# Kernel tuning notes

Measured on AMD Instinct MI355X. Metric: run time of the kernel, lower is better.

The kernel has to match this reference:

```python
import jax, jax.numpy as jnp
import numpy as np

EPS_MAG = 1e-6    # magnitude threshold for valid trajectory
EPS_WSUM = 1e-8   # clamp on combined weight sum


def setup_inputs() -> dict:
    key = jax.random.key(0)
    embeddings = jax.random.normal(key, (4, 4096, 1024), dtype=jnp.float32)
    return {"embeddings": embeddings, "max_trajectory_distance": 8}


def reference(embeddings, max_trajectory_distance):
    # Vectorized form of compute_sparse_trajectories:
    # for each pos p >= 1, window of diffs d[start..p-1], start = max(0, p - max_dist),
    # normalized diffs weighted by linspace(0.1, 1.0, window) * tanh(2*|d|),
    # output[p] = weighted sum / clamp(weight sum, 1e-8); output[0] = 0.
    B, S, D = embeddings.shape
    maxd = min(int(max_trajectory_distance), S - 1)

    d = embeddings[:, 1:, :] - embeddings[:, :-1, :]            # [B, S-1, D]
    mag = jnp.linalg.norm(d, axis=-1)                           # [B, S-1]
    normed = jnp.where((mag > EPS_MAG)[..., None],
                       d / jnp.maximum(mag, EPS_MAG)[..., None],
                       0.0)                                     # [B, S-1, D]
    magw = jnp.tanh(mag * 2.0)                                  # [B, S-1]

    p = jnp.arange(S)                                           # positions
    wsize = jnp.minimum(maxd, p)                                # window size per pos
    j = jnp.arange(maxd)
    idx = p[:, None] - maxd + j[None, :]                        # [S, maxd] diff indices (end-aligned)
    valid = idx >= 0                                            # [S, maxd]
    # k = rank within window (0..wsize-1): weights linspace(0.1, 1.0, wsize)
    k = (j[None, :] - (maxd - wsize)[:, None]).astype(jnp.float32)
    denom = jnp.maximum(wsize - 1, 1).astype(jnp.float32)[:, None]
    lin = jnp.where(wsize[:, None] > 1, 0.1 + 0.9 * k / denom, 0.1)
    lin = jnp.where(valid, lin, 0.0)                            # [S, maxd]

    ci = jnp.clip(idx, 0, S - 2)                                # safe gather indices
    n_g = normed[:, ci, :]                                      # [B, S, maxd, D]
    m_g = magw[:, ci]                                           # [B, S, maxd]
    comb = lin[None, :, :] * m_g * valid[None, :, :]            # combined weights

    wsum = jnp.maximum(comb.sum(axis=-1), EPS_WSUM)             # [B, S]
    traj = jnp.einsum('bsjd,bsj->bsd', n_g, comb) / wsum[..., None]
    return traj
```

## Files before the change

### kernel.cpp

```cpp
#include <hip/hip_runtime.h>
#include <hip/hip_bf16.h>


constexpr int B_ = 4;
constexpr int S_ = 4096;
constexpr int D_ = 1024;
constexpr int MAXD  = 8;
constexpr int CHUNK = 32;
constexpr int ROWS  = CHUNK + MAXD;
constexpr int NDIFF = ROWS - 1;
constexpr int NCH   = S_ / CHUNK;
constexpr int NWG   = B_ * NCH;
constexpr int NXCD  = 8;

typedef float fx4 __attribute__((ext_vector_type(4)));

template <int CTRL, int ROW_MASK>
__device__ __forceinline__ float dpp_add(float x) {
    const int t = __builtin_amdgcn_update_dpp(0, __float_as_int(x),
                                              CTRL, ROW_MASK, 0xf, false);
    return x + __int_as_float(t);
}

__device__ __forceinline__ float wave_reduce_dpp(float x) {
    x = dpp_add<0x111, 0xf>(x);
    x = dpp_add<0x112, 0xf>(x);
    x = dpp_add<0x114, 0xf>(x);
    x = dpp_add<0x118, 0xf>(x);
    x = dpp_add<0x142, 0xa>(x);
    x = dpp_add<0x143, 0xc>(x);
    return x;
}

__global__ __launch_bounds__(256, 2)
void traj_splat_kernel(const float* __restrict__ emb, float* __restrict__ out) {
    const int bid = blockIdx.x;
    const int lin = (bid % NXCD) * (NWG / NXCD) + bid / NXCD;
    const int schunk = lin & (NCH - 1);
    const int b      = lin >> 7;

    const int s0   = schunk * CHUNK;
    const int lane = threadIdx.x & 63;
    const int wave = threadIdx.x >> 6;
    const int d0   = threadIdx.x * 4;

    const float* __restrict__ embB = emb + (size_t)b * S_ * D_;

    __shared__ float part[NDIFF][5];
    __shared__ float smagw[NDIFF];
    __shared__ float sq[NDIFF];
    __shared__ float gco[CHUNK][12];

    float4 win[ROWS];
    #pragma unroll
    for (int r = 0; r < ROWS; ++r) {
        const int row = s0 - MAXD + r;
        win[r] = (row >= 0) ? *(const float4*)(embB + (size_t)row * D_ + d0)
                            : make_float4(0.f, 0.f, 0.f, 0.f);
    }

    #pragma unroll
    for (int li = 0; li < NDIFF; ++li) {
        const float4 a = win[li], c = win[li + 1];
        const float dx = c.x - a.x, dy = c.y - a.y;
        const float dz = c.z - a.z, dw = c.w - a.w;
        float sum = dx * dx + dy * dy + dz * dz + dw * dw;
        sum = wave_reduce_dpp(sum);
        if (lane == 63) part[li][wave] = sum;
    }
    __syncthreads();

    if (threadIdx.x < NDIFF) {
        const int li = threadIdx.x;
        const float s2 = part[li][0] + part[li][1] + part[li][2] + part[li][3];
        const float mag = sqrtf(s2);
        const float mw  = tanhf(2.f * mag);
        smagw[li] = mw;
        sq[li]    = (mag > 1e-6f) ? (mw / mag) : 0.f;
    }
    __syncthreads();

    if (threadIdx.x < CHUNK) {
        const int sl = threadIdx.x;
        const int s  = s0 + sl;
        const int ws = min(MAXD, s);
        const int lo = MAXD - ws;
        const float rden = 0.9f / (float)max(ws - 1, 1);

        float cpad[MAXD + 2];
        #pragma unroll
        for (int t = 0; t < MAXD + 2; ++t) cpad[t] = 0.f;

        float wsum = 0.f;
        #pragma unroll
        for (int j = 0; j < MAXD; ++j) {
            if (j >= lo) {
                const int li = sl + j;
                const float lin2 = (ws > 1) ? (0.1f + rden * (float)(j - lo)) : 0.1f;
                wsum += lin2 * smagw[li];
                cpad[j + 1] = lin2 * sq[li];
            }
        }
        const float inv = 1.f / fmaxf(wsum, 1e-8f);
        #pragma unroll
        for (int jr = 0; jr <= MAXD; ++jr)
            gco[sl][jr] = (cpad[jr] - cpad[jr + 1]) * inv;
    }
    __syncthreads();

    float* outB = out + ((size_t)b * S_ + s0) * D_ + d0;
    #pragma unroll
    for (int sl = 0; sl < CHUNK; ++sl) {
        const float4 g0 = *(const float4*)&gco[sl][0];
        const float4 g1 = *(const float4*)&gco[sl][4];
        const float  g8 = gco[sl][8];

        float ax = g0.x * win[sl].x;
        float ay = g0.x * win[sl].y;
        float az = g0.x * win[sl].z;
        float aw = g0.x * win[sl].w;
        const float gs[8] = {g0.y, g0.z, g0.w, g1.x, g1.y, g1.z, g1.w, g8};
        #pragma unroll
        for (int jr = 1; jr <= MAXD; ++jr) {
            const float g = gs[jr - 1];
            ax += g * win[sl + jr].x;
            ay += g * win[sl + jr].y;
            az += g * win[sl + jr].z;
            aw += g * win[sl + jr].w;
        }
        fx4 acc4; acc4.x = ax; acc4.y = ay; acc4.z = az; acc4.w = aw;
        __builtin_nontemporal_store(acc4, (fx4*)(outB + (size_t)sl * D_));
    }
}

extern "C" void kernel_launch(void* const* d_in, const int* in_sizes, int n_in,
                              void* d_out, int out_size, void* d_ws, size_t ws_size,
                              hipStream_t stream) {
    const float* emb = (const float*)d_in[0];
    float* out = (float*)d_out;

    dim3 grid(NWG);
    dim3 block(256);
    traj_splat_kernel<<<grid, block, 0, stream>>>(emb, out);
}
```

Baseline: 25.93 us.

## Replace block barriers with per-wave redundant coefficient computation

Each of the four waves now recomputes the magnitude, tanh weight and splat coefficients into its own LDS slice after one block barrier. This drops two of the three __syncthreads in favour of wave-local lgkmcnt fences, removing cross-wave waits between the small serial phases. In exchange every wave repeats the scalar coefficient work and uses four times the LDS for those arrays, and correctness relies on lockstep execution within a wave plus the explicit waitcnt fences.

```diff
diff --git a/kernel.cpp b/kernel.cpp
--- a/kernel.cpp
+++ b/kernel.cpp
@@ -12,6 +12,7 @@
 constexpr int NCH   = S_ / CHUNK;
 constexpr int NWG   = B_ * NCH;
 constexpr int NXCD  = 8;
+constexpr int NWAVE = 4;
 
 typedef float fx4 __attribute__((ext_vector_type(4)));
 
@@ -32,6 +33,11 @@
     return x;
 }
 
+__device__ __forceinline__ void wave_lds_fence() {
+    asm volatile("s_waitcnt lgkmcnt(0)" ::: "memory");
+    __builtin_amdgcn_sched_barrier(0);
+}
+
 __global__ __launch_bounds__(256, 2)
 void traj_splat_kernel(const float* __restrict__ emb, float* __restrict__ out) {
     const int bid = blockIdx.x;
@@ -47,9 +53,9 @@
     const float* __restrict__ embB = emb + (size_t)b * S_ * D_;
 
     __shared__ float part[NDIFF][5];
-    __shared__ float smagw[NDIFF];
-    __shared__ float sq[NDIFF];
-    __shared__ float gco[CHUNK][12];
+    __shared__ float smagw[NWAVE][NDIFF + 1];
+    __shared__ float sq[NWAVE][NDIFF + 1];
+    __shared__ float gco[NWAVE][CHUNK][12];
 
     float4 win[ROWS];
     #pragma unroll
@@ -68,20 +74,22 @@
         sum = wave_reduce_dpp(sum);
         if (lane == 63) part[li][wave] = sum;
     }
-    __syncthreads();
 
-    if (threadIdx.x < NDIFF) {
-        const int li = threadIdx.x;
-        const float s2 = part[li][0] + part[li][1] + part[li][2] + part[li][3];
+    asm volatile("s_waitcnt lgkmcnt(0)" ::: "memory");
+    __builtin_amdgcn_s_barrier();
+
+    if (lane < NDIFF) {
+        const float s2 = part[lane][0] + part[lane][1]
+                       + part[lane][2] + part[lane][3];
         const float mag = sqrtf(s2);
         const float mw  = tanhf(2.f * mag);
-        smagw[li] = mw;
-        sq[li]    = (mag > 1e-6f) ? (mw / mag) : 0.f;
+        smagw[wave][lane] = mw;
+        sq[wave][lane]    = (mag > 1e-6f) ? (mw / mag) : 0.f;
     }
-    __syncthreads();
+    wave_lds_fence();
 
-    if (threadIdx.x < CHUNK) {
-        const int sl = threadIdx.x;
+    if (lane < CHUNK) {
+        const int sl = lane;
         const int s  = s0 + sl;
         const int ws = min(MAXD, s);
         const int lo = MAXD - ws;
@@ -97,23 +105,23 @@
             if (j >= lo) {
                 const int li = sl + j;
                 const float lin2 = (ws > 1) ? (0.1f + rden * (float)(j - lo)) : 0.1f;
-                wsum += lin2 * smagw[li];
-                cpad[j + 1] = lin2 * sq[li];
+                wsum += lin2 * smagw[wave][li];
+                cpad[j + 1] = lin2 * sq[wave][li];
             }
         }
         const float inv = 1.f / fmaxf(wsum, 1e-8f);
         #pragma unroll
         for (int jr = 0; jr <= MAXD; ++jr)
-            gco[sl][jr] = (cpad[jr] - cpad[jr + 1]) * inv;
+            gco[wave][sl][jr] = (cpad[jr] - cpad[jr + 1]) * inv;
     }
-    __syncthreads();
+    wave_lds_fence();
 
     float* outB = out + ((size_t)b * S_ + s0) * D_ + d0;
     #pragma unroll
     for (int sl = 0; sl < CHUNK; ++sl) {
-        const float4 g0 = *(const float4*)&gco[sl][0];
-        const float4 g1 = *(const float4*)&gco[sl][4];
-        const float  g8 = gco[sl][8];
+        const float4 g0 = *(const float4*)&gco[wave][sl][0];
+        const float4 g1 = *(const float4*)&gco[wave][sl][4];
+        const float  g8 = gco[wave][sl][8];
 
         float ax = g0.x * win[sl].x;
         float ay = g0.x * win[sl].y;
```

New measurement: 25.95 us. No clear change (+0.1%).
